# Optimization experiments

Hardware: AMD Instinct MI355X
Metric: run time of the kernel (lower is better)

The kernel has to match this reference:

```python
import jax, jax.numpy as jnp
import numpy as np

D_MODEL = 1024
N_HEADS = 16
HEAD_DIM = D_MODEL // N_HEADS
D_FF = 4096
RANK = 8
B, T = 4, 2048


def _layernorm(x, g, b, eps=1e-5):
    mu = jnp.mean(x, axis=-1, keepdims=True)
    var = jnp.var(x, axis=-1, keepdims=True)
    return (x - mu) * jax.lax.rsqrt(var + eps) * g + b


def _dyn_linear(x, W, A, b_dyn, bias=None):
    # base: x [b,t,i] @ W.T  (W is [o,i] like nn.Linear)
    out = jnp.einsum('bti,oi->bto', x, W)
    if bias is not None:
        out = out + bias
    # per-sample low-rank delta: (x @ b_dyn.T) @ A.T
    delta = jnp.einsum('bti,bri,or->bto', x, b_dyn, A)
    return out + delta


def setup_inputs() -> dict:
    key = jax.random.key(0)
    ks = jax.random.split(key, 24)
    s = 0.02
    inp = {
        'x': jax.random.normal(ks[0], (B, T, D_MODEL), jnp.float32),
        'dyn_q': jax.random.normal(ks[1], (B, RANK, D_MODEL), jnp.float32) * s,
        'dyn_k': jax.random.normal(ks[2], (B, RANK, D_MODEL), jnp.float32) * s,
        'dyn_v': jax.random.normal(ks[3], (B, RANK, D_MODEL), jnp.float32) * s,
        'dyn_ff1': jax.random.normal(ks[4], (B, RANK, D_MODEL), jnp.float32) * s,
        'dyn_ff2': jax.random.normal(ks[5], (B, RANK, D_FF), jnp.float32) * s,
        'Wq': jax.random.normal(ks[6], (D_MODEL, D_MODEL), jnp.float32) / np.sqrt(D_MODEL),
        'Aq': jax.random.normal(ks[7], (D_MODEL, RANK), jnp.float32) * s,
        'Wk': jax.random.normal(ks[8], (D_MODEL, D_MODEL), jnp.float32) / np.sqrt(D_MODEL),
        'Ak': jax.random.normal(ks[9], (D_MODEL, RANK), jnp.float32) * s,
        'Wv': jax.random.normal(ks[10], (D_MODEL, D_MODEL), jnp.float32) / np.sqrt(D_MODEL),
        'Av': jax.random.normal(ks[11], (D_MODEL, RANK), jnp.float32) * s,
        'Wo': jax.random.normal(ks[12], (D_MODEL, D_MODEL), jnp.float32) / np.sqrt(D_MODEL),
        'W1': jax.random.normal(ks[13], (D_FF, D_MODEL), jnp.float32) / np.sqrt(D_MODEL),
        'b1': jnp.zeros((D_FF,), jnp.float32),
        'A1': jax.random.normal(ks[14], (D_FF, RANK), jnp.float32) * s,
        'W2': jax.random.normal(ks[15], (D_MODEL, D_FF), jnp.float32) / np.sqrt(D_FF),
        'b2': jnp.zeros((D_MODEL,), jnp.float32),
        'A2': jax.random.normal(ks[16], (D_MODEL, RANK), jnp.float32) * s,
        'g1': jnp.ones((D_MODEL,), jnp.float32),
        'beta1': jnp.zeros((D_MODEL,), jnp.float32),
        'g2': jnp.ones((D_MODEL,), jnp.float32),
        'beta2': jnp.zeros((D_MODEL,), jnp.float32),
    }
    return inp


def reference(x, dyn_q, dyn_k, dyn_v, dyn_ff1, dyn_ff2,
              Wq, Aq, Wk, Ak, Wv, Av, Wo,
              W1, b1, A1, W2, b2, A2,
              g1, beta1, g2, beta2):
    bsz, seq_len, _ = x.shape
    residual = x
    h = _layernorm(x, g1, beta1)
    q = _dyn_linear(h, Wq, Aq, dyn_q)
    k = _dyn_linear(h, Wk, Ak, dyn_k)
    v = _dyn_linear(h, Wv, Av, dyn_v)
    # [b, t, h, d] -> [b, h, t, d]
    q = q.reshape(bsz, seq_len, N_HEADS, HEAD_DIM).transpose(0, 2, 1, 3)
    k = k.reshape(bsz, seq_len, N_HEADS, HEAD_DIM).transpose(0, 2, 1, 3)
    v = v.reshape(bsz, seq_len, N_HEADS, HEAD_DIM).transpose(0, 2, 1, 3)
    score = jnp.einsum('bhqd,bhkd->bhqk', q, k) / np.sqrt(HEAD_DIM).astype(np.float32)
    attn = jax.nn.softmax(score, axis=-1)
    ctx = jnp.einsum('bhqk,bhkd->bhqd', attn, v)
    ctx = ctx.transpose(0, 2, 1, 3).reshape(bsz, seq_len, D_MODEL)
    x = residual + jnp.einsum('bti,oi->bto', ctx, Wo)  # dropout p=0
    residual = x
    h = _layernorm(x, g2, beta2)
    ff = jax.nn.gelu(_dyn_linear(h, W1, A1, dyn_ff1, bias=b1), approximate=False)
    ff = _dyn_linear(ff, W2, A2, dyn_ff2, bias=b2)
    return residual + ff
```

## Files before the change

### kernel.cpp

```cpp
#include <hip/hip_runtime.h>
#include <math.h>

#define D_MODEL 1024
#define D_FF    4096
#define RANK    8
#define BATCH   4
#define SEQ     2048
#define MTOT    (BATCH*SEQ)
#define NHEADS  16
#define HDIM    64

typedef __attribute__((ext_vector_type(8))) __bf16 bf16x8;
typedef __attribute__((ext_vector_type(4))) float f32x4;
typedef __attribute__((ext_vector_type(8))) unsigned short u16x8;
typedef __attribute__((ext_vector_type(4))) unsigned short u16x4;

__device__ __forceinline__ unsigned short f2bf(float f) {
  __bf16 h = (__bf16)f;
  return __builtin_bit_cast(unsigned short, h);
}
__device__ __forceinline__ float bf2f(unsigned short h) {
  union { unsigned int u; float f; } v; v.u = ((unsigned int)h) << 16;
  return v.f;
}

__device__ __forceinline__ f32x4 mfma16(bf16x8 a, bf16x8 b, f32x4 c) {
  return __builtin_amdgcn_mfma_f32_16x16x32_bf16(a, b, c, 0, 0, 0);
}

#define GLDS(g, l) __builtin_amdgcn_global_load_lds( \
    (const __attribute__((address_space(1))) void*)(g), \
    (__attribute__((address_space(3))) void*)(l), 16, 0, 0)

__global__ __launch_bounds__(256) void cvt_bf16_all(
    const float* __restrict__ s0, const float* __restrict__ s1,
    const float* __restrict__ s2, const float* __restrict__ s3,
    const float* __restrict__ s4, const float* __restrict__ s5,
    unsigned short* __restrict__ d0, unsigned short* __restrict__ d1,
    unsigned short* __restrict__ d2, unsigned short* __restrict__ d3,
    unsigned short* __restrict__ d4, unsigned short* __restrict__ d5)
{
  const int b = blockIdx.x;
  const float* src; unsigned short* dst; int base;
  if (b < 512)       { src = s0; dst = d0; base = b; }
  else if (b < 1024) { src = s1; dst = d1; base = b - 512; }
  else if (b < 1536) { src = s2; dst = d2; base = b - 1024; }
  else if (b < 2048) { src = s3; dst = d3; base = b - 1536; }
  else if (b < 4096) { src = s4; dst = d4; base = b - 2048; }
  else               { src = s5; dst = d5; base = b - 4096; }
  const size_t i = (size_t)base * 256 + threadIdx.x;
  const float4 a  = *reinterpret_cast<const float4*>(src + i * 8);
  const float4 c  = *reinterpret_cast<const float4*>(src + i * 8 + 4);
  u16x8 o;
  o[0] = f2bf(a.x); o[1] = f2bf(a.y); o[2] = f2bf(a.z); o[3] = f2bf(a.w);
  o[4] = f2bf(c.x); o[5] = f2bf(c.y); o[6] = f2bf(c.z); o[7] = f2bf(c.w);
  *reinterpret_cast<u16x8*>(dst + i * 8) = o;
}

__global__ __launch_bounds__(256) void ln_fwd(const float* __restrict__ x,
                                              const float* __restrict__ g,
                                              const float* __restrict__ be,
                                              unsigned short* __restrict__ out)
{
  const int row = blockIdx.x;
  const int t = threadIdx.x;
  const float* xr = x + (size_t)row * D_MODEL;
  float4 vv = *reinterpret_cast<const float4*>(xr + t * 4);
  float s  = vv.x + vv.y + vv.z + vv.w;
  float s2 = vv.x * vv.x + vv.y * vv.y + vv.z * vv.z + vv.w * vv.w;
#pragma unroll
  for (int mm = 1; mm < 64; mm <<= 1) { s += __shfl_xor(s, mm); s2 += __shfl_xor(s2, mm); }
  __shared__ float red[8];
  const int w = t >> 6, l = t & 63;
  if (l == 0) { red[w] = s; red[4 + w] = s2; }
  __syncthreads();
  s  = red[0] + red[1] + red[2] + red[3];
  s2 = red[4] + red[5] + red[6] + red[7];
  float mean = s * (1.f / D_MODEL);
  float var  = s2 * (1.f / D_MODEL) - mean * mean;
  float rstd = rsqrtf(var + 1e-5f);
  float4 gv = *reinterpret_cast<const float4*>(g  + t * 4);
  float4 bv = *reinterpret_cast<const float4*>(be + t * 4);
  u16x4 o;
  o[0] = f2bf((vv.x - mean) * rstd * gv.x + bv.x);
  o[1] = f2bf((vv.y - mean) * rstd * gv.y + bv.y);
  o[2] = f2bf((vv.z - mean) * rstd * gv.z + bv.z);
  o[3] = f2bf((vv.w - mean) * rstd * gv.w + bv.w);
  *reinterpret_cast<u16x4*>(out + (size_t)row * D_MODEL + t * 4) = o;
}

template<int ILEN>
__global__ __launch_bounds__(256) void dyn_u(const unsigned short* __restrict__ hmat,
                                             const float* __restrict__ dyn,
                                             float* __restrict__ u)
{
  const int tid = threadIdx.x, w = tid >> 6, l = tid & 63;
  const int m0 = blockIdx.x * 16 + w * 4;
  const int b = m0 / SEQ;
  const float* dynb = dyn + (size_t)b * RANK * ILEN;
  float acc[4][RANK] = {};
  for (int s = 0; s < ILEN / 64; ++s) {
    const int i = l + s * 64;
    float hv[4];
#pragma unroll
    for (int rr = 0; rr < 4; ++rr) hv[rr] = bf2f(hmat[(size_t)(m0 + rr) * ILEN + i]);
#pragma unroll
    for (int r = 0; r < RANK; ++r) {
      float d = dynb[(size_t)r * ILEN + i];
#pragma unroll
      for (int rr = 0; rr < 4; ++rr) acc[rr][r] += hv[rr] * d;
    }
  }
#pragma unroll
  for (int rr = 0; rr < 4; ++rr)
#pragma unroll
    for (int r = 0; r < RANK; ++r) {
      float a = acc[rr][r];
#pragma unroll
      for (int mm = 1; mm < 64; mm <<= 1) a += __shfl_xor(a, mm);
      if (l == 0) u[(size_t)(m0 + rr) * RANK + r] = a;
    }
}

__global__ __launch_bounds__(256) void dyn_u_qkv(const unsigned short* __restrict__ hmat,
                                                 const float* __restrict__ dq,
                                                 const float* __restrict__ dk,
                                                 const float* __restrict__ dv,
                                                 float* __restrict__ u)
{
  const int tid = threadIdx.x, w = tid >> 6, l = tid & 63;
  const int m0 = blockIdx.x * 16 + w * 4;
  const int b = m0 / SEQ;
  const float* db0 = dq + (size_t)b * RANK * D_MODEL;
  const float* db1 = dk + (size_t)b * RANK * D_MODEL;
  const float* db2 = dv + (size_t)b * RANK * D_MODEL;
  float acc[4][3 * RANK] = {};
  for (int s = 0; s < D_MODEL / 64; ++s) {
    const int i = l + s * 64;
    float hv[4];
#pragma unroll
    for (int rr = 0; rr < 4; ++rr) hv[rr] = bf2f(hmat[(size_t)(m0 + rr) * D_MODEL + i]);
#pragma unroll
    for (int r = 0; r < RANK; ++r) {
      float d0 = db0[(size_t)r * D_MODEL + i];
      float d1 = db1[(size_t)r * D_MODEL + i];
      float d2 = db2[(size_t)r * D_MODEL + i];
#pragma unroll
      for (int rr = 0; rr < 4; ++rr) {
        acc[rr][r] += hv[rr] * d0;
        acc[rr][RANK + r] += hv[rr] * d1;
        acc[rr][2 * RANK + r] += hv[rr] * d2;
      }
    }
  }
#pragma unroll
  for (int g = 0; g < 3; ++g)
#pragma unroll
    for (int rr = 0; rr < 4; ++rr)
#pragma unroll
      for (int r = 0; r < RANK; ++r) {
        float a = acc[rr][g * RANK + r];
#pragma unroll
        for (int mm = 1; mm < 64; mm <<= 1) a += __shfl_xor(a, mm);
        if (l == 0) u[((size_t)g * MTOT + m0 + rr) * RANK + r] = a;
      }
}

template<int NDIM, int KDIM, int MODE, int BN>
__global__ __launch_bounds__(512, (BN == 256) ? 1 : 2)
void gemm_bt(const unsigned short* __restrict__ A,
             const unsigned short* __restrict__ B,
             void* __restrict__ outp,
             void* __restrict__ outp2,
             const float* __restrict__ uvec,
             const float* __restrict__ Ad0,
             const float* __restrict__ Ad1,
             const float* __restrict__ Ad2,
             const float* __restrict__ bias,
             const float* __restrict__ resid)
{
  constexpr bool HAS_DYN = (MODE == 2 || MODE == 3 || MODE == 5);
  constexpr int WN = BN / 64;
  constexpr int WM = 8 / WN;
  constexpr int MSPAN = 256 / WM;
  constexpr int NI = MSPAN / 16;
  __shared__ unsigned short sAB[2][(256 + BN) * 64];
  const int tid = threadIdx.x;
  const int w = tid >> 6, l = tid & 63;

  constexpr int NBX = NDIM / BN;
  constexpr int NWG = NBX * (MTOT / 256);
  const int bid = blockIdx.y * NBX + blockIdx.x;
  const int sbid = (bid & 7) * (NWG / 8) + (bid >> 3);
  const int tm = (sbid / NBX) * 256, tn = (sbid % NBX) * BN;
  const int wm = w / WN, wn = w % WN;

  f32x4 acc[NI][4] = {};

  const int srow = l >> 3;
  const int sc8 = (l & 7) ^ (srow & 7);
  const unsigned short* Ag = A + (size_t)(tm + srow) * KDIM + sc8 * 8;
  const unsigned short* Bg = B + (size_t)(tn + srow) * KDIM + sc8 * 8;

  const int arow = wm * MSPAN + (l & 15);
  const int bcol = wn * 64 + (l & 15);
  const int kb0 = l >> 4;
  const int swz = l & 7;

  constexpr int NT = KDIM / 64;

  auto stage = [&](int buf, int kt) {
    unsigned short* bA = &sAB[buf][0];
    unsigned short* bB = &sAB[buf][256 * 64];
#pragma unroll
    for (int it = 0; it < 4; ++it) {
      const int st = w * 4 + it;
      GLDS(Ag + (size_t)(st * 8) * KDIM + kt, bA + st * 512);
    }
#pragma unroll
    for (int it = 0; it < WN; ++it) {
      const int st = w * WN + it;
      GLDS(Bg + (size_t)(st * 8) * KDIM + kt, bB + st * 512);
    }
  };

  stage(0, 0);
  asm volatile("s_waitcnt vmcnt(0)" ::: "memory");
  __syncthreads();

  int cur = 0;
  for (int t = 0; t < NT; ++t) {
    if (t + 1 < NT) stage(cur ^ 1, (t + 1) * 64);

    const unsigned short* sA_ = &sAB[cur][0];
    const unsigned short* sB_ = &sAB[cur][256 * 64];
#pragma unroll
    for (int kk = 0; kk < 2; ++kk) {
      bf16x8 af[NI], bfv[4];
      const int kphys = ((kk * 4 + kb0) ^ swz) << 3;
#pragma unroll
      for (int i = 0; i < NI; ++i)
        af[i] = *reinterpret_cast<const bf16x8*>(&sA_[(arow + i * 16) * 64 + kphys]);
#pragma unroll
      for (int j = 0; j < 4; ++j)
        bfv[j] = *reinterpret_cast<const bf16x8*>(&sB_[(bcol + j * 16) * 64 + kphys]);
#pragma unroll
      for (int i = 0; i < NI; ++i)
#pragma unroll
        for (int j = 0; j < 4; ++j)
          acc[i][j] = mfma16(af[i], bfv[j], acc[i][j]);
    }
    __syncthreads();
    cur ^= 1;
  }

  const int rbase = tm + wm * MSPAN + ((l >> 4) << 2);
  const int cbase = tn + wn * 64 + (l & 15);

  const int seg = tn >> 10;
  const float* Ad = Ad0;
  const float* uv = uvec;
  if constexpr (MODE == 5) {
    Ad = (seg == 0) ? Ad0 : (seg == 1) ? Ad1 : Ad2;
    uv = uvec + (size_t)seg * ((size_t)MTOT * RANK);
  }

#pragma unroll
  for (int i = 0; i < NI; ++i) {
    float uu[4][8];
    if constexpr (HAS_DYN) {
#pragma unroll
      for (int r = 0; r < 4; ++r) {
        const float* up = uv + (size_t)(rbase + i * 16 + r) * RANK;
#pragma unroll
        for (int p = 0; p < 8; ++p) uu[r][p] = up[p];
      }
    }
#pragma unroll
    for (int j = 0; j < 4; ++j) {
      const int col = cbase + j * 16;
      float ad[8];
      if constexpr (HAS_DYN) {
#pragma unroll
        for (int p = 0; p < 8; ++p) ad[p] = Ad[(size_t)col * RANK + p];
      }
      float vv4[4];
#pragma unroll
      for (int r = 0; r < 4; ++r) {
        const int row = rbase + i * 16 + r;
        float v = acc[i][j][r];
        if constexpr (HAS_DYN) {
#pragma unroll
          for (int p = 0; p < 8; ++p) v += uu[r][p] * ad[p];
        }
        if constexpr (MODE == 2) {
          v += bias[col];
          v = 0.5f * v * (1.f + erff(v * 0.70710678118654752f));
        }
        if constexpr (MODE == 1) {
          v += resid[(size_t)row * NDIM + col];
        }
        if constexpr (MODE == 3) {
          v += bias[col] + resid[(size_t)row * NDIM + col];
        }
        if constexpr (MODE == 5) {
          if (seg == 0) v *= 0.18033688011112042f;
        }
        vv4[r] = v;
      }
      if constexpr (MODE == 2) {
#pragma unroll
        for (int r = 0; r < 4; ++r)
          ((unsigned short*)outp)[(size_t)(rbase + i * 16 + r) * NDIM + col] = f2bf(vv4[r]);
      } else if constexpr (MODE == 5) {
        const int cl = col & 1023;
        if (seg < 2) {
#pragma unroll
          for (int r = 0; r < 4; ++r)
            ((unsigned short*)outp)[((size_t)seg * MTOT + rbase + i * 16 + r) * D_MODEL + cl] =
                f2bf(vv4[r]);
        } else {
          const int row0 = rbase + i * 16;
          const int bb = row0 >> 11, t0 = row0 & (SEQ - 1);
          const int hh = cl >> 6, dd = cl & 63;
          const int jj = (t0 >> 4) & 3;
          unsigned short* vb = &((unsigned short*)outp2)[
              (((size_t)bb * NHEADS + hh) * HDIM + dd) * SEQ + (t0 & ~63)];
#pragma unroll
          for (int dlt = 0; dlt < 4; ++dlt)
            vb[((t0 & 15) + dlt) * 4 + jj] = f2bf(vv4[dlt]);
        }
      } else {
#pragma unroll
        for (int r = 0; r < 4; ++r)
          ((float*)outp)[(size_t)(rbase + i * 16 + r) * NDIM + col] = vv4[r];
      }
    }
  }
}

__global__ __launch_bounds__(256, 4) void attn_fwd(const unsigned short* __restrict__ q,
                                                   const unsigned short* __restrict__ k,
                                                   const unsigned short* __restrict__ vt,
                                                   unsigned short* __restrict__ ctx)
{
  __shared__ unsigned short sK[128 * 64];
  __shared__ unsigned short sV[64 * 128];
  __shared__ unsigned short sP[4][32 * 64];

  const int tid = threadIdx.x, w = tid >> 6, l = tid & 63;
  const int lin = blockIdx.y * (SEQ / 128) + blockIdx.x;
  const int W = (lin & 7) * ((BATCH * NHEADS * SEQ / 128) / 8) + (lin >> 3);
  const int bh = W >> 4, b = bh >> 4, hh = bh & 15;
  const int q0 = (W & 15) * 128 + w * 32;
  const size_t base = ((size_t)b * SEQ) * D_MODEL + hh * HDIM;
  const size_t vtbase = (size_t)bh * HDIM * SEQ;

  bf16x8 qf[2][2];
#pragma unroll
  for (int i = 0; i < 2; ++i)
#pragma unroll
    for (int ks = 0; ks < 2; ++ks)
      qf[i][ks] = *reinterpret_cast<const bf16x8*>(
          &q[base + (size_t)(q0 + i * 16 + (l & 15)) * D_MODEL + ks * 32 + (l >> 4) * 8]);

  float mrun[2][4], lrun[2][4];
  f32x4 oacc[2][4] = {};
#pragma unroll
  for (int i = 0; i < 2; ++i)
#pragma unroll
    for (int r = 0; r < 4; ++r) { mrun[i][r] = -3.0e38f; lrun[i][r] = 0.f; }

  const int krow_l = l >> 3;
  const int kswz = (l & 7) ^ (krow_l & 7);
  const unsigned short* kg = k + base + (size_t)krow_l * D_MODEL + kswz * 8;
  const int vrow_l = l >> 4;
  const int vswz = (l & 15) ^ (((w & 1) * 4 + vrow_l) & 7);
  const unsigned short* vg = vt + vtbase + (size_t)vrow_l * SEQ + vswz * 8;

  const int swz = l & 7;
  const int kb0 = l >> 4;

  for (int kt = 0; kt < SEQ; kt += 128) {
    __syncthreads();
#pragma unroll
    for (int it = 0; it < 4; ++it) {
      const int r4 = it * 4 + w;
      GLDS(kg + (size_t)(kt + r4 * 8) * D_MODEL, sK + r4 * 512);
      GLDS(vg + (size_t)(r4 * 4) * SEQ + kt, sV + r4 * 512);
    }
    asm volatile("s_waitcnt vmcnt(0)" ::: "memory");
    __syncthreads();

    f32x4 sacc[2][8] = {};
    __builtin_amdgcn_s_setprio(1);
#pragma unroll
    for (int ks = 0; ks < 2; ++ks) {
#pragma unroll
      for (int j = 0; j < 8; ++j) {
        const int row = j * 16 + (l & 15);
        bf16x8 kf = *reinterpret_cast<const bf16x8*>(
            &sK[row * 64 + (((ks * 4 + kb0) ^ swz) << 3)]);
#pragma unroll
        for (int i = 0; i < 2; ++i) sacc[i][j] = mfma16(qf[i][ks], kf, sacc[i][j]);
      }
    }
    __builtin_amdgcn_s_setprio(0);

    float pr[2][4][4];
    const int c15 = l & 15;
#pragma unroll
    for (int i = 0; i < 2; ++i) {
#pragma unroll
      for (int r = 0; r < 4; ++r) {
        float sv[8];
#pragma unroll
        for (int j = 0; j < 8; ++j) sv[j] = sacc[i][j][r];
        float mx = fmaxf(fmaxf(fmaxf(sv[0], sv[1]), fmaxf(sv[2], sv[3])),
                         fmaxf(fmaxf(sv[4], sv[5]), fmaxf(sv[6], sv[7])));
#pragma unroll
        for (int mm = 1; mm < 16; mm <<= 1) mx = fmaxf(mx, __shfl_xor(mx, mm, 16));
        const float mnew = fmaxf(mrun[i][r], mx);
        const float alpha = __builtin_exp2f(mrun[i][r] - mnew);
        mrun[i][r] = mnew;
        float p[8], ps = 0.f;
#pragma unroll
        for (int j = 0; j < 8; ++j) { p[j] = __builtin_exp2f(sv[j] - mnew); ps += p[j]; }
#pragma unroll
        for (int mm = 1; mm < 16; mm <<= 1) ps += __shfl_xor(ps, mm, 16);
        lrun[i][r] = lrun[i][r] * alpha + ps;
        const int prow = i * 16 + ((l >> 4) << 2) + r;
        u16x4 pk;
        pk[0] = f2bf(p[0]); pk[1] = f2bf(p[1]); pk[2] = f2bf(p[2]); pk[3] = f2bf(p[3]);
        *reinterpret_cast<u16x4*>(
            &sP[w][prow * 64 + ((((c15 >> 1) ^ (prow & 7)) << 3) | ((c15 & 1) << 2))]) = pk;
#pragma unroll
        for (int jj = 0; jj < 4; ++jj) pr[i][r][jj] = p[4 + jj];
#pragma unroll
        for (int j = 0; j < 4; ++j) oacc[i][j][r] *= alpha;
      }
    }

    __builtin_amdgcn_s_setprio(1);
#pragma unroll
    for (int ks = 0; ks < 2; ++ks) {
      bf16x8 pf[2];
#pragma unroll
      for (int i = 0; i < 2; ++i) {
        const int prw = i * 16 + (l & 15);
        pf[i] = *reinterpret_cast<const bf16x8*>(
            &sP[w][prw * 64 + (((ks * 4 + kb0) ^ (prw & 7)) << 3)]);
      }
#pragma unroll
      for (int j = 0; j < 4; ++j) {
        const int row = j * 16 + (l & 15);
        bf16x8 vf = *reinterpret_cast<const bf16x8*>(
            &sV[row * 128 + (((ks * 4 + kb0) ^ swz) << 3)]);
#pragma unroll
        for (int i = 0; i < 2; ++i) oacc[i][j] = mfma16(pf[i], vf, oacc[i][j]);
      }
    }
    __builtin_amdgcn_s_setprio(0);

#pragma unroll
    for (int i = 0; i < 2; ++i) {
#pragma unroll
      for (int r = 0; r < 4; ++r) {
        const int prow = i * 16 + ((l >> 4) << 2) + r;
        u16x4 pk;
        pk[0] = f2bf(pr[i][r][0]); pk[1] = f2bf(pr[i][r][1]);
        pk[2] = f2bf(pr[i][r][2]); pk[3] = f2bf(pr[i][r][3]);
        *reinterpret_cast<u16x4*>(
            &sP[w][prow * 64 + ((((c15 >> 1) ^ (prow & 7)) << 3) | ((c15 & 1) << 2))]) = pk;
      }
    }

    __builtin_amdgcn_s_setprio(1);
#pragma unroll
    for (int ks = 0; ks < 2; ++ks) {
      bf16x8 pf[2];
#pragma unroll
      for (int i = 0; i < 2; ++i) {
        const int prw = i * 16 + (l & 15);
        pf[i] = *reinterpret_cast<const bf16x8*>(
            &sP[w][prw * 64 + (((ks * 4 + kb0) ^ (prw & 7)) << 3)]);
      }
#pragma unroll
      for (int j = 0; j < 4; ++j) {
        const int row = j * 16 + (l & 15);
        bf16x8 vf = *reinterpret_cast<const bf16x8*>(
            &sV[row * 128 + (((8 + ks * 4 + kb0) ^ swz) << 3)]);
#pragma unroll
        for (int i = 0; i < 2; ++i) oacc[i][j] = mfma16(pf[i], vf, oacc[i][j]);
      }
    }
    __builtin_amdgcn_s_setprio(0);
  }

#pragma unroll
  for (int i = 0; i < 2; ++i)
#pragma unroll
    for (int r = 0; r < 4; ++r) {
      float inv = 1.f / lrun[i][r];
      int row = q0 + i * 16 + ((l >> 4) << 2) + r;
#pragma unroll
      for (int j = 0; j < 4; ++j)
        ctx[base + (size_t)row * D_MODEL + j * 16 + (l & 15)] = f2bf(oacc[i][j][r] * inv);
    }
}

extern "C" void kernel_launch(void* const* d_in, const int* in_sizes, int n_in,
                              void* d_out, int out_size, void* d_ws, size_t ws_size,
                              hipStream_t stream)
{
  (void)in_sizes; (void)n_in; (void)out_size; (void)ws_size;
  const float* x      = (const float*)d_in[0];
  const float* dyn_q  = (const float*)d_in[1];
  const float* dyn_k  = (const float*)d_in[2];
  const float* dyn_v  = (const float*)d_in[3];
  const float* dyn_f1 = (const float*)d_in[4];
  const float* dyn_f2 = (const float*)d_in[5];
  const float* Wq = (const float*)d_in[6];
  const float* Aq = (const float*)d_in[7];
  const float* Wk = (const float*)d_in[8];
  const float* Ak = (const float*)d_in[9];
  const float* Wv = (const float*)d_in[10];
  const float* Av = (const float*)d_in[11];
  const float* Wo = (const float*)d_in[12];
  const float* W1 = (const float*)d_in[13];
  const float* b1 = (const float*)d_in[14];
  const float* A1 = (const float*)d_in[15];
  const float* W2 = (const float*)d_in[16];
  const float* b2 = (const float*)d_in[17];
  const float* A2 = (const float*)d_in[18];
  const float* g1 = (const float*)d_in[19];
  const float* be1 = (const float*)d_in[20];
  const float* g2 = (const float*)d_in[21];
  const float* be2 = (const float*)d_in[22];

  char* ws = (char*)d_ws;
  size_t o = 0;
  auto take = [&](size_t b) { size_t r = o; o += (b + 255) & ~(size_t)255; return r; };
  const size_t o_wq = take((size_t)D_MODEL * D_MODEL * 2);
  const size_t o_wk = take((size_t)D_MODEL * D_MODEL * 2);
  const size_t o_wv = take((size_t)D_MODEL * D_MODEL * 2);
  const size_t o_wo = take((size_t)D_MODEL * D_MODEL * 2);
  const size_t o_w1 = take((size_t)D_FF * D_MODEL * 2);
  const size_t o_w2 = take((size_t)D_FF * D_MODEL * 2);
  const size_t o_h1 = take((size_t)MTOT * D_MODEL * 2);
  const size_t o_q  = take((size_t)MTOT * D_MODEL * 2);
  const size_t o_k  = take((size_t)MTOT * D_MODEL * 2);
  const size_t o_v  = take((size_t)MTOT * D_MODEL * 2);
  const size_t o_u  = take((size_t)MTOT * RANK * 4 * 3);
  const size_t o_ff = take((size_t)MTOT * D_FF * 2);

  unsigned short* wq_b = (unsigned short*)(ws + o_wq);
  unsigned short* wk_b = (unsigned short*)(ws + o_wk);
  unsigned short* wv_b = (unsigned short*)(ws + o_wv);
  unsigned short* wo_b = (unsigned short*)(ws + o_wo);
  unsigned short* w1_b = (unsigned short*)(ws + o_w1);
  unsigned short* w2_b = (unsigned short*)(ws + o_w2);
  unsigned short* h1   = (unsigned short*)(ws + o_h1);
  unsigned short* qb   = (unsigned short*)(ws + o_q);
  unsigned short* vtb  = (unsigned short*)(ws + o_v);
  float* u_q  = (float*)(ws + o_u);
  float* u_k  = u_q + (size_t)MTOT * RANK;
  unsigned short* ctx = h1;
  float* x2 = (float*)(ws + o_q);
  unsigned short* h2 = vtb;
  float* u_f1 = u_q;
  float* u_f2 = u_k;
  unsigned short* ffb = (unsigned short*)(ws + o_ff);

  cvt_bf16_all<<<6144, 256, 0, stream>>>(Wq, Wk, Wv, Wo, W1, W2,
                                         wq_b, wk_b, wv_b, wo_b, w1_b, w2_b);

  ln_fwd<<<MTOT, 256, 0, stream>>>(x, g1, be1, h1);

  dyn_u_qkv<<<MTOT / 16, 256, 0, stream>>>(h1, dyn_q, dyn_k, dyn_v, u_q);

  gemm_bt<3 * D_MODEL, D_MODEL, 5, 256><<<dim3(3 * D_MODEL / 256, MTOT / 256), 512, 0, stream>>>(
      h1, wq_b, qb, vtb, u_q, Aq, Ak, Av, nullptr, nullptr);

  attn_fwd<<<dim3(SEQ / 128, BATCH * NHEADS), 256, 0, stream>>>(
      qb, qb + (size_t)MTOT * D_MODEL, vtb, ctx);

  gemm_bt<D_MODEL, D_MODEL, 1, 128><<<dim3(D_MODEL / 128, MTOT / 256), 512, 0, stream>>>(
      ctx, wo_b, x2, nullptr, nullptr, nullptr, nullptr, nullptr, nullptr, x);

  ln_fwd<<<MTOT, 256, 0, stream>>>(x2, g2, be2, h2);

  dyn_u<D_MODEL><<<MTOT / 16, 256, 0, stream>>>(h2, dyn_f1, u_f1);
  gemm_bt<D_FF, D_MODEL, 2, 256><<<dim3(D_FF / 256, MTOT / 256), 512, 0, stream>>>(
      h2, w1_b, ffb, nullptr, u_f1, A1, nullptr, nullptr, b1, nullptr);

  dyn_u<D_FF><<<MTOT / 16, 256, 0, stream>>>(ffb, dyn_f2, u_f2);
  gemm_bt<D_MODEL, D_FF, 3, 128><<<dim3(D_MODEL / 128, MTOT / 256), 512, 0, stream>>>(
      ffb, w2_b, (float*)d_out, nullptr, u_f2, A2, nullptr, nullptr, b2, x2);
}
```

Before: 619.5 us.

## Add 8-phase pipelined 256x256 GEMM kernel for QKV and FF1 projections

Adds a new gemm8p kernel that splits each 256x256 tile into four 128x128 quadrants. It runs eight barrier-separated MFMA phases per two K-tiles, interleaving global-to-LDS loads for later tiles with the math and raising wave priority during the MFMA bursts. It is meant to hide load latency and LDS barrier stalls in the large-N GEMMs (QKV and FF1). The old gemm_bt epilogue is split so that its specialization keeps only the float-output modes, and the new kernel handles the bf16 modes. The cost is a fixed manual waitcnt and barrier schedule that is fragile and uses heavy LDS (128KB) with 2 blocks per CU.

```diff
diff --git a/kernel.cpp b/kernel.cpp
--- a/kernel.cpp
+++ b/kernel.cpp
@@ -257,6 +257,139 @@
   const int rbase = tm + wm * MSPAN + ((l >> 4) << 2);
   const int cbase = tn + wn * 64 + (l & 15);
 
+#pragma unroll
+  for (int i = 0; i < NI; ++i) {
+    float uu[4][8];
+    if constexpr (HAS_DYN) {
+#pragma unroll
+      for (int r = 0; r < 4; ++r) {
+        const float* up = uvec + (size_t)(rbase + i * 16 + r) * RANK;
+#pragma unroll
+        for (int p = 0; p < 8; ++p) uu[r][p] = up[p];
+      }
+    }
+#pragma unroll
+    for (int j = 0; j < 4; ++j) {
+      const int col = cbase + j * 16;
+      float ad[8];
+      if constexpr (HAS_DYN) {
+#pragma unroll
+        for (int p = 0; p < 8; ++p) ad[p] = Ad0[(size_t)col * RANK + p];
+      }
+      float vv4[4];
+#pragma unroll
+      for (int r = 0; r < 4; ++r) {
+        const int row = rbase + i * 16 + r;
+        float v = acc[i][j][r];
+        if constexpr (HAS_DYN) {
+#pragma unroll
+          for (int p = 0; p < 8; ++p) v += uu[r][p] * ad[p];
+        }
+        if constexpr (MODE == 1) {
+          v += resid[(size_t)row * NDIM + col];
+        }
+        if constexpr (MODE == 3) {
+          v += bias[col] + resid[(size_t)row * NDIM + col];
+        }
+        vv4[r] = v;
+      }
+#pragma unroll
+      for (int r = 0; r < 4; ++r)
+        ((float*)outp)[(size_t)(rbase + i * 16 + r) * NDIM + col] = vv4[r];
+    }
+  }
+}
+
+#define PHASE8(BUF, MS, NS, STAGE, VMW) {                                     \
+  bf16x8 afr[4][2], bfr[2][2];                                                \
+  _Pragma("unroll") for (int kk = 0; kk < 2; ++kk) {                          \
+    const int kp = ((kk * 4 + kb0) ^ swz) << 3;                               \
+    _Pragma("unroll") for (int mf = 0; mf < 4; ++mf)                          \
+      afr[mf][kk] = *reinterpret_cast<const bf16x8*>(                         \
+          &sA[BUF][MS][(wm * 64 + mf * 16 + (l & 15)) * 64 + kp]);            \
+    _Pragma("unroll") for (int nf = 0; nf < 2; ++nf)                          \
+      bfr[nf][kk] = *reinterpret_cast<const bf16x8*>(                         \
+          &sB[BUF][NS][(wn * 32 + nf * 16 + (l & 15)) * 64 + kp]);            \
+  }                                                                           \
+  STAGE                                                                       \
+  asm volatile("s_barrier" ::: "memory");                                     \
+  __builtin_amdgcn_sched_barrier(0);                                          \
+  __builtin_amdgcn_s_setprio(1);                                              \
+  _Pragma("unroll") for (int kk = 0; kk < 2; ++kk)                            \
+    _Pragma("unroll") for (int mf = 0; mf < 4; ++mf)                          \
+      _Pragma("unroll") for (int nf = 0; nf < 2; ++nf)                        \
+        acc[MS * 4 + mf][NS * 2 + nf] =                                       \
+            mfma16(afr[mf][kk], bfr[nf][kk], acc[MS * 4 + mf][NS * 2 + nf]);  \
+  __builtin_amdgcn_s_setprio(0);                                              \
+  VMW                                                                         \
+  asm volatile("s_barrier" ::: "memory"); }
+
+#define VM4 asm volatile("s_waitcnt vmcnt(4)" ::: "memory");
+
+template<int NDIM, int KDIM, int MODE>
+__global__ __launch_bounds__(512, 2)
+void gemm8p(const unsigned short* __restrict__ A,
+            const unsigned short* __restrict__ B,
+            void* __restrict__ outp,
+            void* __restrict__ outp2,
+            const float* __restrict__ uvec,
+            const float* __restrict__ Ad0,
+            const float* __restrict__ Ad1,
+            const float* __restrict__ Ad2,
+            const float* __restrict__ bias,
+            const float* __restrict__ resid)
+{
+  __shared__ unsigned short sA[2][2][128 * 64];
+  __shared__ unsigned short sB[2][2][128 * 64];
+  const int tid = threadIdx.x, w = tid >> 6, l = tid & 63;
+
+  constexpr int NBX = NDIM / 256;
+  constexpr int NWG = NBX * (MTOT / 256);
+  const int bid = blockIdx.y * NBX + blockIdx.x;
+  const int sbid = (bid & 7) * (NWG / 8) + (bid >> 3);
+  const int tm = (sbid / NBX) * 256, tn = (sbid % NBX) * 256;
+  const int wm = w >> 2, wn = w & 3;
+
+  f32x4 acc[8][4] = {};
+
+  const unsigned short* Agl = A + (size_t)(tm + (l >> 3)) * KDIM + ((l & 7) ^ (l >> 3)) * 8;
+  const unsigned short* Bgl = B + (size_t)(tn + (l >> 3)) * KDIM + ((l & 7) ^ (l >> 3)) * 8;
+
+  const int kb0 = l >> 4, swz = l & 7;
+
+  auto stA = [&](int buf, int half, int T) {
+#pragma unroll
+    for (int g = 0; g < 2; ++g) {
+      const int c = g * 8 + w;
+      GLDS(Agl + (size_t)(half * 128 + c * 8) * KDIM + T * 64, &sA[buf][half][c * 512]);
+    }
+  };
+  auto stB = [&](int buf, int half, int T) {
+#pragma unroll
+    for (int g = 0; g < 2; ++g) {
+      const int c = g * 8 + w;
+      GLDS(Bgl + (size_t)(half * 128 + c * 8) * KDIM + T * 64, &sB[buf][half][c * 512]);
+    }
+  };
+
+  constexpr int NT = KDIM / 64;
+
+  stA(0, 0, 0); stB(0, 0, 0); stA(0, 1, 0); stB(0, 1, 0);
+  stA(1, 0, 1); stB(1, 0, 1);
+  asm volatile("s_waitcnt vmcnt(4)" ::: "memory");
+  asm volatile("s_barrier" ::: "memory");
+
+  for (int T = 0; T < NT; T += 2) {
+    PHASE8(0, 0, 0, stA(1, 1, T + 1);, )
+    PHASE8(0, 0, 1, stB(1, 1, T + 1);, )
+    PHASE8(0, 1, 0, if (T + 2 < NT) { stA(0, 0, T + 2); }, )
+    PHASE8(0, 1, 1, if (T + 2 < NT) { stB(0, 0, T + 2); }, VM4)
+    PHASE8(1, 0, 0, if (T + 2 < NT) { stA(0, 1, T + 2); }, )
+    PHASE8(1, 0, 1, if (T + 2 < NT) { stB(0, 1, T + 2); }, )
+    PHASE8(1, 1, 0, if (T + 3 < NT) { stA(1, 0, T + 3); }, )
+    PHASE8(1, 1, 1, if (T + 3 < NT) { stB(1, 0, T + 3); }, VM4)
+  }
+
   const int seg = tn >> 10;
   const float* Ad = Ad0;
   const float* uv = uvec;
@@ -266,42 +399,30 @@
   }
 
 #pragma unroll
-  for (int i = 0; i < NI; ++i) {
+  for (int i = 0; i < 8; ++i) {
+    const int rb = tm + (i >> 2) * 128 + wm * 64 + (i & 3) * 16 + ((l >> 4) << 2);
     float uu[4][8];
-    if constexpr (HAS_DYN) {
+#pragma unroll
+    for (int r = 0; r < 4; ++r) {
+      const float* up = uv + (size_t)(rb + r) * RANK;
+#pragma unroll
+      for (int p = 0; p < 8; ++p) uu[r][p] = up[p];
+    }
+#pragma unroll
+    for (int j = 0; j < 4; ++j) {
+      const int col = tn + (j >> 1) * 128 + wn * 32 + (j & 1) * 16 + (l & 15);
+      float ad[8];
+#pragma unroll
+      for (int p = 0; p < 8; ++p) ad[p] = Ad[(size_t)col * RANK + p];
+      float vv4[4];
 #pragma unroll
       for (int r = 0; r < 4; ++r) {
-        const float* up = uv + (size_t)(rbase + i * 16 + r) * RANK;
-#pragma unroll
-        for (int p = 0; p < 8; ++p) uu[r][p] = up[p];
-      }
-    }
-#pragma unroll
-    for (int j = 0; j < 4; ++j) {
-      const int col = cbase + j * 16;
-      float ad[8];
-      if constexpr (HAS_DYN) {
-#pragma unroll
-        for (int p = 0; p < 8; ++p) ad[p] = Ad[(size_t)col * RANK + p];
-      }
-      float vv4[4];
-#pragma unroll
-      for (int r = 0; r < 4; ++r) {
-        const int row = rbase + i * 16 + r;
         float v = acc[i][j][r];
-        if constexpr (HAS_DYN) {
-#pragma unroll
-          for (int p = 0; p < 8; ++p) v += uu[r][p] * ad[p];
-        }
+#pragma unroll
+        for (int p = 0; p < 8; ++p) v += uu[r][p] * ad[p];
         if constexpr (MODE == 2) {
           v += bias[col];
           v = 0.5f * v * (1.f + erff(v * 0.70710678118654752f));
-        }
-        if constexpr (MODE == 1) {
-          v += resid[(size_t)row * NDIM + col];
-        }
-        if constexpr (MODE == 3) {
-          v += bias[col] + resid[(size_t)row * NDIM + col];
         }
         if constexpr (MODE == 5) {
           if (seg == 0) v *= 0.18033688011112042f;
@@ -311,17 +432,16 @@
       if constexpr (MODE == 2) {
 #pragma unroll
         for (int r = 0; r < 4; ++r)
-          ((unsigned short*)outp)[(size_t)(rbase + i * 16 + r) * NDIM + col] = f2bf(vv4[r]);
-      } else if constexpr (MODE == 5) {
+          ((unsigned short*)outp)[(size_t)(rb + r) * NDIM + col] = f2bf(vv4[r]);
+      } else {
         const int cl = col & 1023;
         if (seg < 2) {
 #pragma unroll
           for (int r = 0; r < 4; ++r)
-            ((unsigned short*)outp)[((size_t)seg * MTOT + rbase + i * 16 + r) * D_MODEL + cl] =
+            ((unsigned short*)outp)[((size_t)seg * MTOT + rb + r) * D_MODEL + cl] =
                 f2bf(vv4[r]);
         } else {
-          const int row0 = rbase + i * 16;
-          const int bb = row0 >> 11, t0 = row0 & (SEQ - 1);
+          const int bb = rb >> 11, t0 = rb & (SEQ - 1);
           const int hh = cl >> 6, dd = cl & 63;
           const int jj = (t0 >> 4) & 3;
           unsigned short* vb = &((unsigned short*)outp2)[
@@ -330,10 +450,6 @@
           for (int dlt = 0; dlt < 4; ++dlt)
             vb[((t0 & 15) + dlt) * 4 + jj] = f2bf(vv4[dlt]);
         }
-      } else {
-#pragma unroll
-        for (int r = 0; r < 4; ++r)
-          ((float*)outp)[(size_t)(rbase + i * 16 + r) * NDIM + col] = vv4[r];
       }
     }
   }
@@ -579,7 +695,7 @@
 
   dyn_u_qkv<<<MTOT / 16, 256, 0, stream>>>(h1, dyn_q, dyn_k, dyn_v, u_q);
 
-  gemm_bt<3 * D_MODEL, D_MODEL, 5, 256><<<dim3(3 * D_MODEL / 256, MTOT / 256), 512, 0, stream>>>(
+  gemm8p<3 * D_MODEL, D_MODEL, 5><<<dim3(3 * D_MODEL / 256, MTOT / 256), 512, 0, stream>>>(
       h1, wq_b, qb, vtb, u_q, Aq, Ak, Av, nullptr, nullptr);
 
   attn_fwd<<<dim3(SEQ / 128, BATCH * NHEADS), 256, 0, stream>>>(
@@ -591,7 +707,7 @@
   ln_fwd<<<MTOT, 256, 0, stream>>>(x2, g2, be2, h2);
 
   dyn_u<D_MODEL><<<MTOT / 16, 256, 0, stream>>>(h2, dyn_f1, u_f1);
-  gemm_bt<D_FF, D_MODEL, 2, 256><<<dim3(D_FF / 256, MTOT / 256), 512, 0, stream>>>(
+  gemm8p<D_FF, D_MODEL, 2><<<dim3(D_FF / 256, MTOT / 256), 512, 0, stream>>>(
       h2, w1_b, ffb, nullptr, u_f1, A1, nullptr, nullptr, b1, nullptr);
 
   dyn_u<D_FF><<<MTOT / 16, 256, 0, stream>>>(ffb, dyn_f2, u_f2);
```

Measured after the change: 627.1 us. No clear change (+1.2%).
